# Performance work log

Measured on AMD Instinct MI355X. Metric: run time of the kernel, lower is better.

The kernel has to match this reference:

```python
import jax, jax.numpy as jnp
import numpy as np

D, E, FF = 512, 8, 4 * 512
BS, H, W = 2, 32, 32
T = BS * H * W


def setup_inputs() -> dict:
    key = jax.random.key(0)
    ks = jax.random.split(key, 12)
    s = lambda fan_in: 1.0 / np.sqrt(fan_in)
    return {
        "x": jax.random.normal(ks[0], (BS, D, H, W), dtype=jnp.float32),
        "Wg": jax.random.normal(ks[1], (D, E), dtype=jnp.float32) * s(D),
        "bg": jnp.zeros((E,), dtype=jnp.float32),
        "Wn": jax.random.normal(ks[2], (D, E), dtype=jnp.float32) * s(D),
        "bn": jnp.zeros((E,), dtype=jnp.float32),
        "W1": jax.random.normal(ks[3], (E, D, FF), dtype=jnp.float32) * s(D),
        "b1": jnp.zeros((E, FF), dtype=jnp.float32),
        "W2": jax.random.normal(ks[4], (E, FF, D), dtype=jnp.float32) * s(FF),
        "b2": jnp.zeros((E, D), dtype=jnp.float32),
        "noise_eps": jax.random.normal(ks[5], (T, E), dtype=jnp.float32),
        "top_k": 2,
    }


def reference(x, Wg, bg, Wn, bn, W1, b1, W2, b2, noise_eps, top_k):
    bs, d, h, w = x.shape
    tokens = x.transpose(0, 2, 3, 1).reshape(-1, d)  # [T, d]
    t = tokens.shape[0]
    # Noisy top-k router
    logits = tokens @ Wg + bg                                  # [T, E]
    noise = noise_eps * jax.nn.softplus(tokens @ Wn + bn)      # [T, E]
    noisy = logits + noise
    top_v, top_i = jax.lax.top_k(noisy, top_k)                 # [T, k]
    sparse = jnp.full_like(noisy, -jnp.inf)
    sparse = sparse.at[jnp.arange(t)[:, None], top_i].set(top_v)
    gates = jax.nn.softmax(sparse, axis=-1)                    # [T, E], zero off top-k
    # Expert MLPs (dense over experts; gates zero-out non-selected)
    hdn = jax.nn.relu(jnp.einsum("td,edf->tef", tokens, W1) + b1)  # [T, E, 4d]
    out_e = jnp.einsum("tef,efd->ted", hdn, W2) + b2               # [T, E, d]
    out = jnp.einsum("te,ted->td", gates, out_e)                   # combine
    return out.reshape(bs, h, w, d).transpose(0, 3, 1, 2)
```

## Files before the change

### kernel.cpp

```cpp
#include <hip/hip_runtime.h>
#include <hip/hip_bf16.h>
#include <math.h>

#define DD  512
#define EE  8
#define FFD 2048
#define TT  2048
#define HWH 1024

typedef __bf16 b16x8 __attribute__((ext_vector_type(8)));
typedef float  f32x4 __attribute__((ext_vector_type(4)));

__device__ __forceinline__ unsigned short f2bf(float f) {
    unsigned u = __builtin_bit_cast(unsigned, f);
    u = (u + 0x7FFFu + ((u >> 16) & 1u)) >> 16;
    return (unsigned short)u;
}

__device__ __forceinline__ void gload16(const void* g, void* l) {
    __builtin_amdgcn_global_load_lds(
        (const __attribute__((address_space(1))) void*)g,
        (__attribute__((address_space(3))) void*)l, 16, 0, 0);
}

__global__ __launch_bounds__(256) void moe_transpose(
    const float* __restrict__ W1, const float* __restrict__ W2,
    const float* __restrict__ x,
    unsigned short* __restrict__ W1t, unsigned short* __restrict__ W2t,
    unsigned short* __restrict__ xb)
{
    int which = blockIdx.z, e = blockIdx.y;
    const float* in; unsigned short* out; int R, C;
    if (which == 0)      { R = DD;  C = FFD; in = W1 + (size_t)e*DD*FFD; out = W1t + (size_t)e*FFD*DD; }
    else if (which == 1) { R = FFD; C = DD;  in = W2 + (size_t)e*FFD*DD; out = W2t + (size_t)e*DD*FFD; }
    else { if (e >= 2) return; R = DD; C = HWH; in = x + (size_t)e*DD*HWH; out = xb + (size_t)e*HWH*DD; }
    int tilesC = C >> 6;
    if ((int)blockIdx.x >= (R >> 6) * tilesC) return;
    int tr = (blockIdx.x / tilesC) << 6, tc = (blockIdx.x % tilesC) << 6;
    __shared__ float ld[64][65];
    int ty = threadIdx.x >> 4, tx = threadIdx.x & 15;
    #pragma unroll
    for (int i = 0; i < 4; ++i) {
        const float4 v = *(const float4*)&in[(size_t)(tr + ty + i*16)*C + tc + tx*4];
        ld[ty + i*16][tx*4+0] = v.x; ld[ty + i*16][tx*4+1] = v.y;
        ld[ty + i*16][tx*4+2] = v.z; ld[ty + i*16][tx*4+3] = v.w;
    }
    __syncthreads();
    #pragma unroll
    for (int i = 0; i < 4; ++i) {
        int c = ty + i*16;
        unsigned o0 = f2bf(ld[tx*4+0][c]) | ((unsigned)f2bf(ld[tx*4+1][c]) << 16);
        unsigned o1 = f2bf(ld[tx*4+2][c]) | ((unsigned)f2bf(ld[tx*4+3][c]) << 16);
        *(uint2*)&out[(size_t)(tc + c)*R + tr + tx*4] = make_uint2(o0, o1);
    }
}

__global__ __launch_bounds__(256) void moe_router_part(
    const float* __restrict__ x, const float* __restrict__ Wg,
    const float* __restrict__ Wn, float* __restrict__ part)
{
    int u = threadIdx.x & 63;
    int q = threadIdx.x >> 6;
    int tt = blockIdx.x, dc = blockIdx.y;
    int t = tt * 64 + u;
    int b = t >> 10, hw = t & 1023;
    const float* xp = x + (size_t)b * DD * HWH + hw;
    int d0 = dc * 64 + q * 16;
    float accL[EE], accN[EE];
    #pragma unroll
    for (int e = 0; e < EE; ++e) { accL[e] = 0.f; accN[e] = 0.f; }
    #pragma unroll
    for (int i = 0; i < 16; ++i) {
        int d = d0 + i;
        float tv = xp[(size_t)d * HWH];
        #pragma unroll
        for (int e = 0; e < EE; ++e) {
            accL[e] = fmaf(tv, Wg[d * EE + e], accL[e]);
            accN[e] = fmaf(tv, Wn[d * EE + e], accN[e]);
        }
    }
    __shared__ float s[4][64][16];
    #pragma unroll
    for (int e = 0; e < EE; ++e) { s[q][u][e] = accL[e]; s[q][u][e + 8] = accN[e]; }
    __syncthreads();
    int idx = threadIdx.x * 4;
    int ot = idx >> 4, oc = idx & 15;
    float4 v;
    v.x = s[0][ot][oc+0] + s[1][ot][oc+0] + s[2][ot][oc+0] + s[3][ot][oc+0];
    v.y = s[0][ot][oc+1] + s[1][ot][oc+1] + s[2][ot][oc+1] + s[3][ot][oc+1];
    v.z = s[0][ot][oc+2] + s[1][ot][oc+2] + s[2][ot][oc+2] + s[3][ot][oc+2];
    v.w = s[0][ot][oc+3] + s[1][ot][oc+3] + s[2][ot][oc+3] + s[3][ot][oc+3];
    *(float4*)&part[((size_t)dc * TT + tt * 64 + ot) * 16 + oc] = v;
}

__global__ __launch_bounds__(256) void moe_router_topk(
    const float* __restrict__ part,
    const float* __restrict__ bg, const float* __restrict__ bn,
    const float* __restrict__ neps,
    int* __restrict__ cnt, int* __restrict__ pair0, int* __restrict__ pair1,
    int* __restrict__ ltok, float* __restrict__ lgate)
{
    int t = blockIdx.x * 256 + threadIdx.x;
    float L[EE], N[EE];
    #pragma unroll
    for (int e = 0; e < EE; ++e) { L[e] = bg[e]; N[e] = bn[e]; }
    #pragma unroll
    for (int dc = 0; dc < 8; ++dc) {
        const float* p = &part[((size_t)dc * TT + t) * 16];
        float4 a0 = *(const float4*)&p[0];
        float4 a1 = *(const float4*)&p[4];
        float4 a2 = *(const float4*)&p[8];
        float4 a3 = *(const float4*)&p[12];
        L[0] += a0.x; L[1] += a0.y; L[2] += a0.z; L[3] += a0.w;
        L[4] += a1.x; L[5] += a1.y; L[6] += a1.z; L[7] += a1.w;
        N[0] += a2.x; N[1] += a2.y; N[2] += a2.z; N[3] += a2.w;
        N[4] += a3.x; N[5] += a3.y; N[6] += a3.z; N[7] += a3.w;
    }
    float noisy[EE];
    #pragma unroll
    for (int e = 0; e < EE; ++e) {
        float sp = fmaxf(N[e], 0.f) + log1pf(expf(-fabsf(N[e])));
        noisy[e] = L[e] + neps[t * EE + e] * sp;
    }
    int e0 = 0; float v0 = noisy[0];
    #pragma unroll
    for (int e = 1; e < EE; ++e) if (noisy[e] > v0) { v0 = noisy[e]; e0 = e; }
    int e1 = (e0 == 0) ? 1 : 0; float v1 = noisy[e1];
    #pragma unroll
    for (int e = 0; e < EE; ++e)
        if (e != e0 && e != e1 && noisy[e] > v1) { v1 = noisy[e]; e1 = e; }
    float ex  = expf(v1 - v0);
    float inv = 1.f / (1.f + ex);
    float g0 = inv, g1 = ex * inv;
    int p0 = atomicAdd(&cnt[e0], 1);
    int p1 = atomicAdd(&cnt[e1], 1);
    ltok[e0 * TT + p0] = t; lgate[e0 * TT + p0] = g0;
    ltok[e1 * TT + p1] = t; lgate[e1 * TT + p1] = g1;
    pair0[t] = (e0 << 16) | p0;
    pair1[t] = (e1 << 16) | p1;
}

__global__ void moe_prefix(const int* __restrict__ cnt, int* __restrict__ seg)
{
    if (threadIdx.x == 0) {
        int s = 0;
        for (int e = 0; e < EE; ++e) { seg[e] = s; s += cnt[e]; }
        seg[EE] = s;
    }
}

__global__ __launch_bounds__(256, 3) void moe_gemm1(
    const unsigned short* __restrict__ xb, const unsigned short* __restrict__ W1t,
    const float* __restrict__ b1, const int* __restrict__ cnt,
    const int* __restrict__ seg, const int* __restrict__ ltok,
    unsigned short* __restrict__ Hbuf)
{
    int e = blockIdx.x, mt = blockIdx.y, nt = blockIdx.z;
    int ce = cnt[e];
    if (mt * 64 >= ce) return;
    int s0 = seg[e];
    const unsigned short* Be = W1t + (size_t)e * FFD * DD;
    __shared__ unsigned short As[2][64 * 64];
    __shared__ unsigned short Bs[2][128 * 64];
    int tid = threadIdx.x, lane = tid & 63, wv = tid >> 6;

    int srow = lane >> 3, schunk = lane & 7;
    int srcoff = ((schunk ^ srow) << 3);

    size_t aoff[2]; int ards[2];
    #pragma unroll
    for (int c = 0; c < 2; ++c) {
        int r0 = (c*4 + wv)*8;
        int ri = mt*64 + r0 + srow;
        int tok = ltok[e * TT + (ri < ce ? ri : 0)];
        aoff[c] = (size_t)tok * DD + srcoff;
        ards[c] = r0 * 64;
    }
    size_t boff[4]; int brds[4];
    #pragma unroll
    for (int c = 0; c < 4; ++c) {
        int r0 = (c*4 + wv)*8;
        boff[c] = (size_t)(nt*128 + r0 + srow) * DD + srcoff;
        brds[c] = r0 * 64;
    }

    int frow = lane & 15, fk = (lane >> 4) * 8;
    int am = (wv >> 1) * 32, bnn = (wv & 1) * 64;
    int rx = (frow & 7) << 3;

    f32x4 acc[2][4];
    f32x4 zero = {0.f, 0.f, 0.f, 0.f};
    #pragma unroll
    for (int m = 0; m < 2; ++m)
        #pragma unroll
        for (int n = 0; n < 4; ++n) acc[m][n] = zero;

    #pragma unroll
    for (int c = 0; c < 2; ++c) gload16(&xb[aoff[c]], &As[0][ards[c]]);
    #pragma unroll
    for (int c = 0; c < 4; ++c) gload16(&Be[boff[c]], &Bs[0][brds[c]]);
    __syncthreads();

    int cur = 0;
    for (int t = 0; t < 8; ++t) {
        if (t < 7) {
            int kk = (t + 1) * 64;
            #pragma unroll
            for (int c = 0; c < 2; ++c) gload16(&xb[aoff[c] + kk], &As[cur^1][ards[c]]);
            #pragma unroll
            for (int c = 0; c < 4; ++c) gload16(&Be[boff[c] + kk], &Bs[cur^1][brds[c]]);
        }
        #pragma unroll
        for (int k2 = 0; k2 < 64; k2 += 32) {
            b16x8 af[2], bf[4];
            #pragma unroll
            for (int m = 0; m < 2; ++m)
                af[m] = *(const b16x8*)&As[cur][(am + m*16 + frow)*64 + ((k2 + fk) ^ rx)];
            #pragma unroll
            for (int n = 0; n < 4; ++n)
                bf[n] = *(const b16x8*)&Bs[cur][(bnn + n*16 + frow)*64 + ((k2 + fk) ^ rx)];
            #pragma unroll
            for (int m = 0; m < 2; ++m)
                #pragma unroll
                for (int n = 0; n < 4; ++n)
                    acc[m][n] = __builtin_amdgcn_mfma_f32_16x16x32_bf16(af[m], bf[n], acc[m][n], 0, 0, 0);
        }
        __syncthreads();
        cur ^= 1;
    }

    int crow = (lane >> 4) * 4;
    #pragma unroll
    for (int m = 0; m < 2; ++m) {
        #pragma unroll
        for (int i = 0; i < 4; ++i) {
            int r = mt*64 + am + m*16 + crow + i;
            if (r < ce) {
                size_t hrow = (size_t)(s0 + r) * FFD;
                #pragma unroll
                for (int n = 0; n < 4; ++n) {
                    int col = nt*128 + bnn + n*16 + frow;
                    float v = acc[m][n][i] + b1[e * FFD + col];
                    Hbuf[hrow + col] = f2bf(fmaxf(v, 0.f));
                }
            }
        }
    }
}

__global__ __launch_bounds__(256, 3) void moe_gemm2(
    const unsigned short* __restrict__ Hbuf, const unsigned short* __restrict__ W2t,
    const int* __restrict__ cnt, const int* __restrict__ seg,
    float* __restrict__ P4)
{
    int e = blockIdx.x, mt = blockIdx.y;
    int split = blockIdx.z >> 2, nt = blockIdx.z & 3;
    int ce = cnt[e];
    if (mt * 64 >= ce) return;
    int s0 = seg[e];
    int kbase = split * 512;
    const unsigned short* Be = W2t + (size_t)e * DD * FFD;
    __shared__ unsigned short As[2][64 * 64];
    __shared__ unsigned short Bs[2][128 * 64];
    int tid = threadIdx.x, lane = tid & 63, wv = tid >> 6;

    int srow = lane >> 3, schunk = lane & 7;
    int srcoff = ((schunk ^ srow) << 3);

    size_t aoff[2]; int ards[2];
    #pragma unroll
    for (int c = 0; c < 2; ++c) {
        int r0 = (c*4 + wv)*8;
        int g = s0 + mt*64 + r0 + srow; if (g > 4095) g = 4095;
        aoff[c] = (size_t)g * FFD + kbase + srcoff;
        ards[c] = r0 * 64;
    }
    size_t boff[4]; int brds[4];
    #pragma unroll
    for (int c = 0; c < 4; ++c) {
        int r0 = (c*4 + wv)*8;
        boff[c] = (size_t)(nt*128 + r0 + srow) * FFD + kbase + srcoff;
        brds[c] = r0 * 64;
    }

    int frow = lane & 15, fk = (lane >> 4) * 8;
    int am = (wv >> 1) * 32, bnn = (wv & 1) * 64;
    int rx = (frow & 7) << 3;

    f32x4 acc[2][4];
    f32x4 zero = {0.f, 0.f, 0.f, 0.f};
    #pragma unroll
    for (int m = 0; m < 2; ++m)
        #pragma unroll
        for (int n = 0; n < 4; ++n) acc[m][n] = zero;

    #pragma unroll
    for (int c = 0; c < 2; ++c) gload16(&Hbuf[aoff[c]], &As[0][ards[c]]);
    #pragma unroll
    for (int c = 0; c < 4; ++c) gload16(&Be[boff[c]], &Bs[0][brds[c]]);
    __syncthreads();

    int cur = 0;
    for (int t = 0; t < 8; ++t) {
        if (t < 7) {
            int kk = (t + 1) * 64;
            #pragma unroll
            for (int c = 0; c < 2; ++c) gload16(&Hbuf[aoff[c] + kk], &As[cur^1][ards[c]]);
            #pragma unroll
            for (int c = 0; c < 4; ++c) gload16(&Be[boff[c] + kk], &Bs[cur^1][brds[c]]);
        }
        #pragma unroll
        for (int k2 = 0; k2 < 64; k2 += 32) {
            b16x8 af[2], bf[4];
            #pragma unroll
            for (int m = 0; m < 2; ++m)
                af[m] = *(const b16x8*)&As[cur][(am + m*16 + frow)*64 + ((k2 + fk) ^ rx)];
            #pragma unroll
            for (int n = 0; n < 4; ++n)
                bf[n] = *(const b16x8*)&Bs[cur][(bnn + n*16 + frow)*64 + ((k2 + fk) ^ rx)];
            #pragma unroll
            for (int m = 0; m < 2; ++m)
                #pragma unroll
                for (int n = 0; n < 4; ++n)
                    acc[m][n] = __builtin_amdgcn_mfma_f32_16x16x32_bf16(af[m], bf[n], acc[m][n], 0, 0, 0);
        }
        __syncthreads();
        cur ^= 1;
    }

    int crow = (lane >> 4) * 4;
    float* Pw = P4 + (size_t)split * 4096 * DD;
    #pragma unroll
    for (int m = 0; m < 2; ++m) {
        #pragma unroll
        for (int i = 0; i < 4; ++i) {
            int r = mt*64 + am + m*16 + crow + i;
            if (r < ce) {
                size_t prow = (size_t)(s0 + r) * DD;
                #pragma unroll
                for (int n = 0; n < 4; ++n) {
                    int col = nt*128 + bnn + n*16 + frow;
                    Pw[prow + col] = acc[m][n][i];
                }
            }
        }
    }
}

__global__ __launch_bounds__(256) void moe_combine(
    const int* __restrict__ pair0, const int* __restrict__ pair1,
    const int* __restrict__ seg, const float* __restrict__ lgate,
    const float* __restrict__ b2, const float* __restrict__ P4,
    float* __restrict__ out)
{
    __shared__ float tile[32][68];
    int tid = threadIdx.x;
    int ti = blockIdx.x, dc = blockIdx.y;
    int ty = tid >> 3, tx = tid & 7;
    int t = ti * 32 + ty;
    int a0 = pair0[t], a1 = pair1[t];
    int e0 = a0 >> 16, sl0 = a0 & 0xFFFF;
    int e1 = a1 >> 16, sl1 = a1 & 0xFFFF;
    int p0 = seg[e0] + sl0, p1 = seg[e1] + sl1;
    float g0 = lgate[e0 * TT + sl0], g1 = lgate[e1 * TT + sl1];
    int d0 = dc * 64 + tx * 8;
    f32x4 s0v[2] = {{0,0,0,0},{0,0,0,0}}, s1v[2] = {{0,0,0,0},{0,0,0,0}};
    #pragma unroll
    for (int s = 0; s < 4; ++s) {
        const f32x4* r0p = (const f32x4*)(P4 + ((size_t)s * 4096 + p0) * DD + d0);
        const f32x4* r1p = (const f32x4*)(P4 + ((size_t)s * 4096 + p1) * DD + d0);
        s0v[0] += r0p[0]; s0v[1] += r0p[1];
        s1v[0] += r1p[0]; s1v[1] += r1p[1];
    }
    const f32x4* b0p = (const f32x4*)(b2 + e0 * DD + d0);
    const f32x4* b1p = (const f32x4*)(b2 + e1 * DD + d0);
    #pragma unroll
    for (int q = 0; q < 2; ++q) {
        f32x4 v = g0 * (s0v[q] + b0p[q]) + g1 * (s1v[q] + b1p[q]);
        *(f32x4*)&tile[ty][tx*8 + q*4] = v;
    }
    __syncthreads();
    int dy = tid >> 2, hx = tid & 3;
    int b = (ti * 32) >> 10, hw0 = (ti * 32) & 1023;
    size_t obase = ((size_t)(b * DD + dc * 64 + dy)) * HWH + hw0;
    #pragma unroll
    for (int q = 0; q < 2; ++q) {
        int j = hx * 8 + q * 4;
        float4 w;
        w.x = tile[j + 0][dy];
        w.y = tile[j + 1][dy];
        w.z = tile[j + 2][dy];
        w.w = tile[j + 3][dy];
        *(float4*)&out[obase + j] = w;
    }
}

extern "C" void kernel_launch(void* const* d_in, const int* in_sizes, int n_in,
                              void* d_out, int out_size, void* d_ws, size_t ws_size,
                              hipStream_t stream)
{
    const float* x    = (const float*)d_in[0];
    const float* Wg   = (const float*)d_in[1];
    const float* bg   = (const float*)d_in[2];
    const float* Wn   = (const float*)d_in[3];
    const float* bn   = (const float*)d_in[4];
    const float* W1   = (const float*)d_in[5];
    const float* b1   = (const float*)d_in[6];
    const float* W2   = (const float*)d_in[7];
    const float* b2   = (const float*)d_in[8];
    const float* neps = (const float*)d_in[9];

    char* ws = (char*)d_ws;
    int*   cnt   = (int*)(ws + 0);
    int*   seg   = (int*)(ws + 256);
    int*   pair0 = (int*)(ws + 512);
    int*   pair1 = (int*)(ws + 8704);
    int*   ltok  = (int*)(ws + 32768);
    float* lgate = (float*)(ws + 98304);
    float* part  = (float*)(ws + 163840);
    unsigned short* xb   = (unsigned short*)(ws + 1212416);
    unsigned short* Hbuf = (unsigned short*)(ws + 3309568);
    unsigned short* W1t  = (unsigned short*)(ws + 20086784);
    unsigned short* W2t  = (unsigned short*)(ws + 36864000);
    float*          P4   = (float*)(ws + 53641216);

    hipMemsetAsync(cnt, 0, 32, stream);
    moe_transpose<<<dim3(256, 8, 3), 256, 0, stream>>>(W1, W2, x, W1t, W2t, xb);
    moe_router_part<<<dim3(TT / 64, 8), 256, 0, stream>>>(x, Wg, Wn, part);
    moe_router_topk<<<TT / 256, 256, 0, stream>>>(part, bg, bn, neps,
                                                  cnt, pair0, pair1, ltok, lgate);
    moe_prefix<<<1, 64, 0, stream>>>(cnt, seg);
    moe_gemm1<<<dim3(EE, 32, 16), 256, 0, stream>>>(xb, W1t, b1, cnt, seg, ltok, Hbuf);
    moe_gemm2<<<dim3(EE, 32, 16), 256, 0, stream>>>(Hbuf, W2t, cnt, seg, P4);
    moe_combine<<<dim3(TT / 32, 8), 256, 0, stream>>>(pair0, pair1, seg, lgate, b2, P4, (float*)d_out);
}
```

Measured before the change: 106.3 us.

## Fuse router into prep kernel, drop prefix kernel, deepen GEMM prefetch pipeline

Merges the router partial-sum kernel into the transpose/convert kernel as an extra grid slice, and removes the prefix-sum kernel by recomputing segment offsets inline from the counts. Both expert GEMMs now keep two K-tiles in flight, using explicit vmcnt waits and raw barriers in place of __syncthreads. The aim is fewer launches and better overlap of global-to-LDS loads with MFMA work. The risks are more redundant count reads per block and fragile hand-written waitcnt accounting.

```diff
diff --git a/kernel.cpp b/kernel.cpp
--- a/kernel.cpp
+++ b/kernel.cpp
@@ -23,13 +23,61 @@
         (__attribute__((address_space(3))) void*)l, 16, 0, 0);
 }
 
-__global__ __launch_bounds__(256) void moe_transpose(
+__device__ __forceinline__ int seg_pred(const int* __restrict__ cnt, int e) {
+    int s = 0;
+    #pragma unroll
+    for (int i = 0; i < EE; ++i) s += (i < e) ? cnt[i] : 0;
+    return s;
+}
+
+__global__ __launch_bounds__(256) void moe_prep(
     const float* __restrict__ W1, const float* __restrict__ W2,
     const float* __restrict__ x,
     unsigned short* __restrict__ W1t, unsigned short* __restrict__ W2t,
-    unsigned short* __restrict__ xb)
-{
+    unsigned short* __restrict__ xb,
+    const float* __restrict__ Wg, const float* __restrict__ Wn,
+    float* __restrict__ part)
+{
+    __shared__ float ld[64][65];
     int which = blockIdx.z, e = blockIdx.y;
+
+    if (which == 3) {
+        if (blockIdx.x >= 32) return;
+        int u = threadIdx.x & 63;
+        int q = threadIdx.x >> 6;
+        int tt = blockIdx.x, dc = e;
+        int t = tt * 64 + u;
+        int b = t >> 10, hw = t & 1023;
+        const float* xp = x + (size_t)b * DD * HWH + hw;
+        int d0 = dc * 64 + q * 16;
+        float accL[EE], accN[EE];
+        #pragma unroll
+        for (int k = 0; k < EE; ++k) { accL[k] = 0.f; accN[k] = 0.f; }
+        #pragma unroll
+        for (int i = 0; i < 16; ++i) {
+            int d = d0 + i;
+            float tv = xp[(size_t)d * HWH];
+            #pragma unroll
+            for (int k = 0; k < EE; ++k) {
+                accL[k] = fmaf(tv, Wg[d * EE + k], accL[k]);
+                accN[k] = fmaf(tv, Wn[d * EE + k], accN[k]);
+            }
+        }
+        float (*s)[64][16] = (float (*)[64][16])&ld[0][0];
+        #pragma unroll
+        for (int k = 0; k < EE; ++k) { s[q][u][k] = accL[k]; s[q][u][k + 8] = accN[k]; }
+        __syncthreads();
+        int idx = threadIdx.x * 4;
+        int ot = idx >> 4, oc = idx & 15;
+        float4 v;
+        v.x = s[0][ot][oc+0] + s[1][ot][oc+0] + s[2][ot][oc+0] + s[3][ot][oc+0];
+        v.y = s[0][ot][oc+1] + s[1][ot][oc+1] + s[2][ot][oc+1] + s[3][ot][oc+1];
+        v.z = s[0][ot][oc+2] + s[1][ot][oc+2] + s[2][ot][oc+2] + s[3][ot][oc+2];
+        v.w = s[0][ot][oc+3] + s[1][ot][oc+3] + s[2][ot][oc+3] + s[3][ot][oc+3];
+        *(float4*)&part[((size_t)dc * TT + tt * 64 + ot) * 16 + oc] = v;
+        return;
+    }
+
     const float* in; unsigned short* out; int R, C;
     if (which == 0)      { R = DD;  C = FFD; in = W1 + (size_t)e*DD*FFD; out = W1t + (size_t)e*FFD*DD; }
     else if (which == 1) { R = FFD; C = DD;  in = W2 + (size_t)e*FFD*DD; out = W2t + (size_t)e*DD*FFD; }
@@ -37,7 +85,6 @@
     int tilesC = C >> 6;
     if ((int)blockIdx.x >= (R >> 6) * tilesC) return;
     int tr = (blockIdx.x / tilesC) << 6, tc = (blockIdx.x % tilesC) << 6;
-    __shared__ float ld[64][65];
     int ty = threadIdx.x >> 4, tx = threadIdx.x & 15;
     #pragma unroll
     for (int i = 0; i < 4; ++i) {
@@ -53,44 +100,6 @@
         unsigned o1 = f2bf(ld[tx*4+2][c]) | ((unsigned)f2bf(ld[tx*4+3][c]) << 16);
         *(uint2*)&out[(size_t)(tc + c)*R + tr + tx*4] = make_uint2(o0, o1);
     }
-}
-
-__global__ __launch_bounds__(256) void moe_router_part(
-    const float* __restrict__ x, const float* __restrict__ Wg,
-    const float* __restrict__ Wn, float* __restrict__ part)
-{
-    int u = threadIdx.x & 63;
-    int q = threadIdx.x >> 6;
-    int tt = blockIdx.x, dc = blockIdx.y;
-    int t = tt * 64 + u;
-    int b = t >> 10, hw = t & 1023;
-    const float* xp = x + (size_t)b * DD * HWH + hw;
-    int d0 = dc * 64 + q * 16;
-    float accL[EE], accN[EE];
-    #pragma unroll
-    for (int e = 0; e < EE; ++e) { accL[e] = 0.f; accN[e] = 0.f; }
-    #pragma unroll
-    for (int i = 0; i < 16; ++i) {
-        int d = d0 + i;
-        float tv = xp[(size_t)d * HWH];
-        #pragma unroll
-        for (int e = 0; e < EE; ++e) {
-            accL[e] = fmaf(tv, Wg[d * EE + e], accL[e]);
-            accN[e] = fmaf(tv, Wn[d * EE + e], accN[e]);
-        }
-    }
-    __shared__ float s[4][64][16];
-    #pragma unroll
-    for (int e = 0; e < EE; ++e) { s[q][u][e] = accL[e]; s[q][u][e + 8] = accN[e]; }
-    __syncthreads();
-    int idx = threadIdx.x * 4;
-    int ot = idx >> 4, oc = idx & 15;
-    float4 v;
-    v.x = s[0][ot][oc+0] + s[1][ot][oc+0] + s[2][ot][oc+0] + s[3][ot][oc+0];
-    v.y = s[0][ot][oc+1] + s[1][ot][oc+1] + s[2][ot][oc+1] + s[3][ot][oc+1];
-    v.z = s[0][ot][oc+2] + s[1][ot][oc+2] + s[2][ot][oc+2] + s[3][ot][oc+2];
-    v.w = s[0][ot][oc+3] + s[1][ot][oc+3] + s[2][ot][oc+3] + s[3][ot][oc+3];
-    *(float4*)&part[((size_t)dc * TT + tt * 64 + ot) * 16 + oc] = v;
 }
 
 __global__ __launch_bounds__(256) void moe_router_topk(
@@ -140,25 +149,15 @@
     pair1[t] = (e1 << 16) | p1;
 }
 
-__global__ void moe_prefix(const int* __restrict__ cnt, int* __restrict__ seg)
-{
-    if (threadIdx.x == 0) {
-        int s = 0;
-        for (int e = 0; e < EE; ++e) { seg[e] = s; s += cnt[e]; }
-        seg[EE] = s;
-    }
-}
-
 __global__ __launch_bounds__(256, 3) void moe_gemm1(
     const unsigned short* __restrict__ xb, const unsigned short* __restrict__ W1t,
     const float* __restrict__ b1, const int* __restrict__ cnt,
-    const int* __restrict__ seg, const int* __restrict__ ltok,
-    unsigned short* __restrict__ Hbuf)
+    const int* __restrict__ ltok, unsigned short* __restrict__ Hbuf)
 {
     int e = blockIdx.x, mt = blockIdx.y, nt = blockIdx.z;
     int ce = cnt[e];
     if (mt * 64 >= ce) return;
-    int s0 = seg[e];
+    int s0 = seg_pred(cnt, e);
     const unsigned short* Be = W1t + (size_t)e * FFD * DD;
     __shared__ unsigned short As[2][64 * 64];
     __shared__ unsigned short Bs[2][128 * 64];
@@ -199,17 +198,18 @@
     for (int c = 0; c < 2; ++c) gload16(&xb[aoff[c]], &As[0][ards[c]]);
     #pragma unroll
     for (int c = 0; c < 4; ++c) gload16(&Be[boff[c]], &Bs[0][brds[c]]);
-    __syncthreads();
-
-    int cur = 0;
+    #pragma unroll
+    for (int c = 0; c < 2; ++c) gload16(&xb[aoff[c] + 64], &As[1][ards[c]]);
+    #pragma unroll
+    for (int c = 0; c < 4; ++c) gload16(&Be[boff[c] + 64], &Bs[1][brds[c]]);
+
+    #pragma unroll
     for (int t = 0; t < 8; ++t) {
-        if (t < 7) {
-            int kk = (t + 1) * 64;
-            #pragma unroll
-            for (int c = 0; c < 2; ++c) gload16(&xb[aoff[c] + kk], &As[cur^1][ards[c]]);
-            #pragma unroll
-            for (int c = 0; c < 4; ++c) gload16(&Be[boff[c] + kk], &Bs[cur^1][brds[c]]);
-        }
+        if (t < 6) { asm volatile("s_waitcnt vmcnt(6)" ::: "memory"); }
+        else       { asm volatile("s_waitcnt vmcnt(0)" ::: "memory"); }
+        __builtin_amdgcn_s_barrier();
+        __builtin_amdgcn_sched_barrier(0);
+        const int cur = t & 1;
         #pragma unroll
         for (int k2 = 0; k2 < 64; k2 += 32) {
             b16x8 af[2], bf[4];
@@ -225,8 +225,14 @@
                 for (int n = 0; n < 4; ++n)
                     acc[m][n] = __builtin_amdgcn_mfma_f32_16x16x32_bf16(af[m], bf[n], acc[m][n], 0, 0, 0);
         }
-        __syncthreads();
-        cur ^= 1;
+        __builtin_amdgcn_s_barrier();
+        if (t < 6) {
+            int kk = (t + 2) * 64;
+            #pragma unroll
+            for (int c = 0; c < 2; ++c) gload16(&xb[aoff[c] + kk], &As[cur][ards[c]]);
+            #pragma unroll
+            for (int c = 0; c < 4; ++c) gload16(&Be[boff[c] + kk], &Bs[cur][brds[c]]);
+        }
     }
 
     int crow = (lane >> 4) * 4;
@@ -250,14 +256,13 @@
 
 __global__ __launch_bounds__(256, 3) void moe_gemm2(
     const unsigned short* __restrict__ Hbuf, const unsigned short* __restrict__ W2t,
-    const int* __restrict__ cnt, const int* __restrict__ seg,
-    float* __restrict__ P4)
+    const int* __restrict__ cnt, float* __restrict__ P4)
 {
     int e = blockIdx.x, mt = blockIdx.y;
     int split = blockIdx.z >> 2, nt = blockIdx.z & 3;
     int ce = cnt[e];
     if (mt * 64 >= ce) return;
-    int s0 = seg[e];
+    int s0 = seg_pred(cnt, e);
     int kbase = split * 512;
     const unsigned short* Be = W2t + (size_t)e * DD * FFD;
     __shared__ unsigned short As[2][64 * 64];
@@ -298,17 +303,18 @@
     for (int c = 0; c < 2; ++c) gload16(&Hbuf[aoff[c]], &As[0][ards[c]]);
     #pragma unroll
     for (int c = 0; c < 4; ++c) gload16(&Be[boff[c]], &Bs[0][brds[c]]);
-    __syncthreads();
-
-    int cur = 0;
+    #pragma unroll
+    for (int c = 0; c < 2; ++c) gload16(&Hbuf[aoff[c] + 64], &As[1][ards[c]]);
+    #pragma unroll
+    for (int c = 0; c < 4; ++c) gload16(&Be[boff[c] + 64], &Bs[1][brds[c]]);
+
+    #pragma unroll
     for (int t = 0; t < 8; ++t) {
-        if (t < 7) {
-            int kk = (t + 1) * 64;
-            #pragma unroll
-            for (int c = 0; c < 2; ++c) gload16(&Hbuf[aoff[c] + kk], &As[cur^1][ards[c]]);
-            #pragma unroll
-            for (int c = 0; c < 4; ++c) gload16(&Be[boff[c] + kk], &Bs[cur^1][brds[c]]);
-        }
+        if (t < 6) { asm volatile("s_waitcnt vmcnt(6)" ::: "memory"); }
+        else       { asm volatile("s_waitcnt vmcnt(0)" ::: "memory"); }
+        __builtin_amdgcn_s_barrier();
+        __builtin_amdgcn_sched_barrier(0);
+        const int cur = t & 1;
         #pragma unroll
         for (int k2 = 0; k2 < 64; k2 += 32) {
             b16x8 af[2], bf[4];
@@ -324,8 +330,14 @@
                 for (int n = 0; n < 4; ++n)
                     acc[m][n] = __builtin_amdgcn_mfma_f32_16x16x32_bf16(af[m], bf[n], acc[m][n], 0, 0, 0);
         }
-        __syncthreads();
-        cur ^= 1;
+        __builtin_amdgcn_s_barrier();
+        if (t < 6) {
+            int kk = (t + 2) * 64;
+            #pragma unroll
+            for (int c = 0; c < 2; ++c) gload16(&Hbuf[aoff[c] + kk], &As[cur][ards[c]]);
+            #pragma unroll
+            for (int c = 0; c < 4; ++c) gload16(&Be[boff[c] + kk], &Bs[cur][brds[c]]);
+        }
     }
 
     int crow = (lane >> 4) * 4;
@@ -349,7 +361,7 @@
 
 __global__ __launch_bounds__(256) void moe_combine(
     const int* __restrict__ pair0, const int* __restrict__ pair1,
-    const int* __restrict__ seg, const float* __restrict__ lgate,
+    const int* __restrict__ cnt, const float* __restrict__ lgate,
     const float* __restrict__ b2, const float* __restrict__ P4,
     float* __restrict__ out)
 {
@@ -361,7 +373,7 @@
     int a0 = pair0[t], a1 = pair1[t];
     int e0 = a0 >> 16, sl0 = a0 & 0xFFFF;
     int e1 = a1 >> 16, sl1 = a1 & 0xFFFF;
-    int p0 = seg[e0] + sl0, p1 = seg[e1] + sl1;
+    int p0 = seg_pred(cnt, e0) + sl0, p1 = seg_pred(cnt, e1) + sl1;
     float g0 = lgate[e0 * TT + sl0], g1 = lgate[e1 * TT + sl1];
     int d0 = dc * 64 + tx * 8;
     f32x4 s0v[2] = {{0,0,0,0},{0,0,0,0}}, s1v[2] = {{0,0,0,0},{0,0,0,0}};
@@ -412,7 +424,6 @@
 
     char* ws = (char*)d_ws;
     int*   cnt   = (int*)(ws + 0);
-    int*   seg   = (int*)(ws + 256);
     int*   pair0 = (int*)(ws + 512);
     int*   pair1 = (int*)(ws + 8704);
     int*   ltok  = (int*)(ws + 32768);
@@ -425,12 +436,10 @@
     float*          P4   = (float*)(ws + 53641216);
 
     hipMemsetAsync(cnt, 0, 32, stream);
-    moe_transpose<<<dim3(256, 8, 3), 256, 0, stream>>>(W1, W2, x, W1t, W2t, xb);
-    moe_router_part<<<dim3(TT / 64, 8), 256, 0, stream>>>(x, Wg, Wn, part);
+    moe_prep<<<dim3(256, 8, 4), 256, 0, stream>>>(W1, W2, x, W1t, W2t, xb, Wg, Wn, part);
     moe_router_topk<<<TT / 256, 256, 0, stream>>>(part, bg, bn, neps,
                                                   cnt, pair0, pair1, ltok, lgate);
-    moe_prefix<<<1, 64, 0, stream>>>(cnt, seg);
-    moe_gemm1<<<dim3(EE, 32, 16), 256, 0, stream>>>(xb, W1t, b1, cnt, seg, ltok, Hbuf);
-    moe_gemm2<<<dim3(EE, 32, 16), 256, 0, stream>>>(Hbuf, W2t, cnt, seg, P4);
-    moe_combine<<<dim3(TT / 32, 8), 256, 0, stream>>>(pair0, pair1, seg, lgate, b2, P4, (float*)d_out);
-}
+    moe_gemm1<<<dim3(EE, 32, 16), 256, 0, stream>>>(xb, W1t, b1, cnt, ltok, Hbuf);
+    moe_gemm2<<<dim3(EE, 32, 16), 256, 0, stream>>>(Hbuf, W2t, cnt, P4);
+    moe_combine<<<dim3(TT / 32, 8), 256, 0, stream>>>(pair0, pair1, cnt, lgate, b2, P4, (float*)d_out);
+}
```

New measurement: 102.0 us. -4.1%, faster.
